# Optimization experiments

Measured on AMD Instinct MI355X. Metric: run time of the kernel, lower is better.

## Reference

```python
import jax, jax.numpy as jnp
import numpy as np

N_NODES = 100000
N_EDGES = 3200000
D_IN = 128
D_OUT = 128


def setup_inputs() -> dict:
    key = jax.random.key(0)
    k1, k2, k3, k4 = jax.random.split(key, 4)
    features = jax.random.normal(k1, (N_NODES, D_IN), dtype=jnp.float32)
    src = jax.random.randint(k2, (N_EDGES,), 0, N_NODES, dtype=jnp.int32)
    dst = jax.random.randint(k3, (N_EDGES,), 0, N_NODES, dtype=jnp.int32)
    # nn.Linear params (Kaiming-uniform-ish init scale)
    bound = 1.0 / np.sqrt(D_IN)
    W = jax.random.uniform(k4, (D_IN, D_OUT), dtype=jnp.float32, minval=-bound, maxval=bound)
    b = jnp.zeros((D_OUT,), dtype=jnp.float32)
    return {"features": features, "W": W, "b": b, "src": src, "dst": dst}


def reference(features, W, b, src, dst):
    # message: gather source node features per edge  [E, D_IN]
    msg = features[src]
    # mean_reduce: segment mean over in-edges per destination node
    summed = jax.ops.segment_sum(msg, dst, num_segments=N_NODES)
    deg = jax.ops.segment_sum(jnp.ones((msg.shape[0],), dtype=features.dtype), dst, num_segments=N_NODES)
    deg = deg[:, None]
    # DGL semantics: nodes with no incoming messages keep their original 'h'
    h = jnp.where(deg > 0, summed / jnp.maximum(deg, 1.0), features)
    # node_update: linear + activation applied to all nodes
    return jax.nn.relu(h @ W + b)
```

## Files before the change

kernel.cpp:

```cpp
#include <hip/hip_runtime.h>

#define N_NODES 100000
#define N_EDGES 3200000
#define D 128

#define BSHIFT 8
#define BSIZE  256
#define NBUCK  391
#define CAP    10240
#define PART_TILE 4096
#define NB_PART ((N_EDGES + PART_TILE - 1) / PART_TILE)
#define CPL 7
#define NSTRIPS (N_NODES / 16)
#define FUSE_GRID 1250

#define OFF_GCUR  0
#define OFF_DBASE 512
#define OFF_OFFS  1024
#define OFF_DEG   101024
#define OFF_CSR   201024
#define FEATB_OFF 13604096ULL
#define WPK_OFF   39204096ULL

typedef __attribute__((ext_vector_type(8))) short short8_t;
typedef __attribute__((ext_vector_type(4))) float f32x4;

__device__ __forceinline__ ushort f2bf(float x) {
    unsigned u = __float_as_uint(x);
    unsigned r = u + 0x7FFFu + ((u >> 16) & 1u);
    return (ushort)(r >> 16);
}
__device__ __forceinline__ float blo(unsigned v) { return __uint_as_float(v << 16); }
__device__ __forceinline__ float bhi(unsigned v) { return __uint_as_float(v & 0xFFFF0000u); }

__global__ __launch_bounds__(256) void gcn_cvt_kernel(
    const float* __restrict__ in, ushort* __restrict__ out, int n8)
{
    int i = blockIdx.x * 256 + threadIdx.x;
    if (i >= n8) return;
    const float4* p = (const float4*)in + (size_t)i * 2;
    float4 a = p[0], b = p[1];
    ushort4 r0 = make_ushort4(f2bf(a.x), f2bf(a.y), f2bf(a.z), f2bf(a.w));
    ushort4 r1 = make_ushort4(f2bf(b.x), f2bf(b.y), f2bf(b.z), f2bf(b.w));
    ushort4* q = (ushort4*)out + (size_t)i * 2;
    q[0] = r0;
    q[1] = r1;
}

__global__ __launch_bounds__(256) void gcn_wpack_kernel(
    const float* __restrict__ W, ushort* __restrict__ wpk)
{
    int tid = blockIdx.x * 256 + threadIdx.x;
    if (tid >= 32 * 64) return;
    int f = tid >> 6, l = tid & 63;
    int n4 = f >> 2, k4 = f & 3;
    int col = n4 * 16 + (l & 15);
    int kb  = k4 * 32 + ((l >> 4) << 3);
    ushort* q = wpk + (size_t)tid * 8;
    #pragma unroll
    for (int t = 0; t < 8; ++t) q[t] = f2bf(W[(kb + t) * D + col]);
}

__global__ void gcn_init_kernel(int* __restrict__ gcur)
{
    int t = blockIdx.x * 256 + threadIdx.x;
    if (t < NBUCK) gcur[t] = t * CAP;
}

__global__ __launch_bounds__(256) void gcn_part_kernel(
    const int* __restrict__ src, const int* __restrict__ dst,
    int* __restrict__ gcur, int* __restrict__ part)
{
    __shared__ int cnt[NBUCK];
    __shared__ int base[NBUCK];
    int t = threadIdx.x;
    for (int i = t; i < NBUCK; i += 256) cnt[i] = 0;
    __syncthreads();

    int eb = blockIdx.x * PART_TILE;
    int dv[PART_TILE / 256], sv[PART_TILE / 256];
    #pragma unroll
    for (int it = 0; it < PART_TILE / 256; ++it) {
        int e = eb + it * 256 + t;
        dv[it] = (e < N_EDGES) ? dst[e] : -1;
        sv[it] = (e < N_EDGES) ? src[e] : 0;
        if (dv[it] >= 0) atomicAdd(&cnt[dv[it] >> BSHIFT], 1);
    }
    __syncthreads();
    for (int i = t; i < NBUCK; i += 256) {
        int c = cnt[i];
        base[i] = c ? atomicAdd(&gcur[i], c) : 0;
        cnt[i] = 0;
    }
    __syncthreads();
    #pragma unroll
    for (int it = 0; it < PART_TILE / 256; ++it) {
        if (dv[it] >= 0) {
            int k  = dv[it] >> BSHIFT;
            int dl = dv[it] & (BSIZE - 1);
            int p  = base[k] + atomicAdd(&cnt[k], 1);
            part[p] = (dl << 17) | sv[it];
        }
    }
}

__global__ __launch_bounds__(64) void gcn_bscan_kernel(
    const int* __restrict__ gcur, int* __restrict__ dbase)
{
    int l = threadIdx.x;
    int v[CPL];
    int s = 0;
    #pragma unroll
    for (int j = 0; j < CPL; ++j) {
        int i = CPL * l + j;
        v[j] = (i < NBUCK) ? (gcur[i] - i * CAP) : 0;
        s += v[j];
    }
    int inc = s;
    #pragma unroll
    for (int d = 1; d < 64; d <<= 1) {
        int up = __shfl_up(inc, d, 64);
        if (l >= d) inc += up;
    }
    int run = inc - s;
    #pragma unroll
    for (int j = 0; j < CPL; ++j) {
        int i = CPL * l + j;
        if (i < NBUCK) dbase[i] = run;
        run += v[j];
    }
}

__global__ __launch_bounds__(256) void gcn_bfill_kernel(
    const int* __restrict__ gcur, const int* __restrict__ dbase,
    const int* __restrict__ part, int* __restrict__ csr,
    int* __restrict__ offs, int* __restrict__ deg)
{
    __shared__ int stage[CAP];
    __shared__ int ldeg[BSIZE];
    __shared__ int lcur[BSIZE];
    __shared__ int wsum[4];
    int k = blockIdx.x, t = threadIdx.x;
    int pb = k * CAP;
    int nE = gcur[k] - pb;
    if (nE > CAP) nE = CAP;
    int db = dbase[k];

    ldeg[t] = 0;
    __syncthreads();
    for (int i = t; i < nE; i += 256) {
        int pk = part[pb + i];
        stage[i] = pk;
        atomicAdd(&ldeg[pk >> 17], 1);
    }
    __syncthreads();

    int lane = t & 63, wid = t >> 6;
    int v = ldeg[t];
    int inc = v;
    #pragma unroll
    for (int d = 1; d < 64; d <<= 1) {
        int up = __shfl_up(inc, d, 64);
        if (lane >= d) inc += up;
    }
    if (lane == 63) wsum[wid] = inc;
    __syncthreads();
    if (t == 0) {
        int c = 0;
        #pragma unroll
        for (int w = 0; w < 4; ++w) { int x = wsum[w]; wsum[w] = c; c += x; }
    }
    __syncthreads();
    int excl = (inc - v) + wsum[wid];
    lcur[t] = excl;
    int node = (k << BSHIFT) + t;
    if (node < N_NODES) { offs[node] = db + excl; deg[node] = v; }
    __syncthreads();

    for (int i = t; i < nE; i += 256) {
        int pk = stage[i];
        int p = atomicAdd(&lcur[pk >> 17], 1);
        csr[db + p] = pk & 0x1FFFF;
    }
}

__global__ __launch_bounds__(256) void gcn_fused_kernel(
    const float* __restrict__ feat,
    const ushort* __restrict__ featb,
    const ushort* __restrict__ wpk,
    const float* __restrict__ bias,
    const int* __restrict__ offs,
    const int* __restrict__ deg,
    const int* __restrict__ csr,
    float* __restrict__ out)
{
    int t = threadIdx.x, lane = t & 63, w = t >> 6;

    short8_t wb[8];
    #pragma unroll
    for (int j = 0; j < 8; ++j)
        wb[j] = *(const short8_t*)(wpk + ((size_t)(w * 8 + j) * 64 + lane) * 8);
    float bj[2];
    bj[0] = bias[(2 * w) * 16 + (lane & 15)];
    bj[1] = bias[(2 * w + 1) * 16 + (lane & 15)];

    __shared__ ushort hlds[16 * 136];

    for (int s = blockIdx.x; s < NSTRIPS; s += FUSE_GRID) {
        int m0 = s * 16;
        __syncthreads();

        #pragma unroll
        for (int i = 0; i < 4; ++i) {
            int r = m0 + w * 4 + i;
            int beg = offs[r], dg = deg[r];
            float s0 = 0.0f, s1 = 0.0f;
            if (dg == 0) {
                float2 f2 = *(const float2*)(feat + (size_t)r * D + lane * 2);
                s0 = f2.x; s1 = f2.y;
            } else {
                int p = beg, e = beg + dg;
                for (; p + 4 <= e; p += 4) {
                    int i0 = csr[p], i1 = csr[p + 1], i2 = csr[p + 2], i3 = csr[p + 3];
                    unsigned v0 = *(const unsigned*)(featb + ((size_t)i0 << 7) + lane * 2);
                    unsigned v1 = *(const unsigned*)(featb + ((size_t)i1 << 7) + lane * 2);
                    unsigned v2 = *(const unsigned*)(featb + ((size_t)i2 << 7) + lane * 2);
                    unsigned v3 = *(const unsigned*)(featb + ((size_t)i3 << 7) + lane * 2);
                    s0 += blo(v0) + blo(v1) + blo(v2) + blo(v3);
                    s1 += bhi(v0) + bhi(v1) + bhi(v2) + bhi(v3);
                }
                for (; p < e; ++p) {
                    unsigned v = *(const unsigned*)(featb + ((size_t)csr[p] << 7) + lane * 2);
                    s0 += blo(v); s1 += bhi(v);
                }
                float inv = 1.0f / (float)dg;
                s0 *= inv; s1 *= inv;
            }
            unsigned pk = ((unsigned)f2bf(s1) << 16) | (unsigned)f2bf(s0);
            *(unsigned*)(&hlds[(w * 4 + i) * 136 + lane * 2]) = pk;
        }
        __syncthreads();

        short8_t a[4];
        #pragma unroll
        for (int k4 = 0; k4 < 4; ++k4)
            a[k4] = *(const short8_t*)(&hlds[(lane & 15) * 136 + k4 * 32 + ((lane >> 4) << 3)]);

        #pragma unroll
        for (int nt = 0; nt < 2; ++nt) {
            f32x4 acc = { bj[nt], bj[nt], bj[nt], bj[nt] };
            #pragma unroll
            for (int k4 = 0; k4 < 4; ++k4)
                acc = __builtin_amdgcn_mfma_f32_16x16x32_bf16(a[k4], wb[nt * 4 + k4], acc, 0, 0, 0);
            int col  = (2 * w + nt) * 16 + (lane & 15);
            int rowb = m0 + ((lane >> 4) << 2);
            #pragma unroll
            for (int rr = 0; rr < 4; ++rr)
                out[(size_t)(rowb + rr) * D + col] = fmaxf(acc[rr], 0.0f);
        }
    }
}

extern "C" void kernel_launch(void* const* d_in, const int* in_sizes, int n_in,
                              void* d_out, int out_size, void* d_ws, size_t ws_size,
                              hipStream_t stream) {
    const float* feat = (const float*)d_in[0];
    const float* W    = (const float*)d_in[1];
    const float* bias = (const float*)d_in[2];
    const int*   src  = (const int*)d_in[3];
    const int*   dst  = (const int*)d_in[4];
    float* out = (float*)d_out;

    int* ib     = (int*)d_ws;
    int* gcur   = ib + OFF_GCUR;
    int* dbase  = ib + OFF_DBASE;
    int* offs   = ib + OFF_OFFS;
    int* deg    = ib + OFF_DEG;
    int* csr    = ib + OFF_CSR;
    ushort* featb = (ushort*)((char*)d_ws + FEATB_OFF);
    ushort* wpk   = (ushort*)((char*)d_ws + WPK_OFF);
    int* part = (int*)d_out;

    {
        int n8 = N_NODES * D / 8;
        gcn_cvt_kernel<<<(n8 + 255) / 256, 256, 0, stream>>>(feat, featb, n8);
    }
    gcn_wpack_kernel<<<8, 256, 0, stream>>>(W, wpk);
    gcn_init_kernel<<<2, 256, 0, stream>>>(gcur);
    gcn_part_kernel<<<NB_PART, 256, 0, stream>>>(src, dst, gcur, part);
    gcn_bscan_kernel<<<1, 64, 0, stream>>>(gcur, dbase);
    gcn_bfill_kernel<<<NBUCK, 256, 0, stream>>>(gcur, dbase, part, csr, offs, deg);
    gcn_fused_kernel<<<FUSE_GRID, 256, 0, stream>>>(feat, featb, wpk, bias, offs, deg, csr, out);
}
```

Measured before the change: 355.9 us.

## Stage partition and CSR fill writes in LDS for coalesced stores; unroll gather by 8

```diff
diff --git a/kernel.cpp b/kernel.cpp
--- a/kernel.cpp
+++ b/kernel.cpp
@@ -7,12 +7,12 @@
 #define BSHIFT 8
 #define BSIZE  256
 #define NBUCK  391
-#define CAP    10240
+#define CAP    9216
 #define PART_TILE 4096
 #define NB_PART ((N_EDGES + PART_TILE - 1) / PART_TILE)
 #define CPL 7
 #define NSTRIPS (N_NODES / 16)
-#define FUSE_GRID 1250
+#define FUSE_GRID 2084
 
 #define OFF_GCUR  0
 #define OFF_DBASE 512
@@ -72,35 +72,76 @@
     int* __restrict__ gcur, int* __restrict__ part)
 {
     __shared__ int cnt[NBUCK];
-    __shared__ int base[NBUCK];
+    __shared__ int lbase[NBUCK + 1];
+    __shared__ int gbase[NBUCK];
+    __shared__ int stage[PART_TILE];
+    __shared__ ushort sbuck[PART_TILE];
+
     int t = threadIdx.x;
+    int eb = blockIdx.x * PART_TILE;
+    int nT = N_EDGES - eb; if (nT > PART_TILE) nT = PART_TILE;
+
     for (int i = t; i < NBUCK; i += 256) cnt[i] = 0;
     __syncthreads();
 
-    int eb = blockIdx.x * PART_TILE;
-    int dv[PART_TILE / 256], sv[PART_TILE / 256];
     #pragma unroll
     for (int it = 0; it < PART_TILE / 256; ++it) {
-        int e = eb + it * 256 + t;
-        dv[it] = (e < N_EDGES) ? dst[e] : -1;
-        sv[it] = (e < N_EDGES) ? src[e] : 0;
-        if (dv[it] >= 0) atomicAdd(&cnt[dv[it] >> BSHIFT], 1);
-    }
-    __syncthreads();
+        int e = it * 256 + t;
+        if (e < nT) atomicAdd(&cnt[dst[eb + e] >> BSHIFT], 1);
+    }
+    __syncthreads();
+
+    if (t < 64) {
+        int v[CPL];
+        int s = 0;
+        #pragma unroll
+        for (int j = 0; j < CPL; ++j) {
+            int i = t * CPL + j;
+            v[j] = (i < NBUCK) ? cnt[i] : 0;
+            s += v[j];
+        }
+        int inc = s;
+        #pragma unroll
+        for (int d = 1; d < 64; d <<= 1) {
+            int up = __shfl_up(inc, d, 64);
+            if (t >= d) inc += up;
+        }
+        int run = inc - s;
+        #pragma unroll
+        for (int j = 0; j < CPL; ++j) {
+            int i = t * CPL + j;
+            if (i < NBUCK) lbase[i] = run;
+            run += v[j];
+        }
+        if (t == 63) lbase[NBUCK] = run;
+    }
+    __syncthreads();
+
     for (int i = t; i < NBUCK; i += 256) {
-        int c = cnt[i];
-        base[i] = c ? atomicAdd(&gcur[i], c) : 0;
+        int c = lbase[i + 1] - lbase[i];
+        gbase[i] = c ? atomicAdd(&gcur[i], c) : 0;
         cnt[i] = 0;
     }
     __syncthreads();
+
     #pragma unroll
     for (int it = 0; it < PART_TILE / 256; ++it) {
-        if (dv[it] >= 0) {
-            int k  = dv[it] >> BSHIFT;
-            int dl = dv[it] & (BSIZE - 1);
-            int p  = base[k] + atomicAdd(&cnt[k], 1);
-            part[p] = (dl << 17) | sv[it];
-        }
+        int e = it * 256 + t;
+        if (e < nT) {
+            int dvv = dst[eb + e];
+            int svv = src[eb + e];
+            int b  = dvv >> BSHIFT;
+            int dl = dvv & (BSIZE - 1);
+            int pos = lbase[b] + atomicAdd(&cnt[b], 1);
+            stage[pos] = (dl << 17) | svv;
+            sbuck[pos] = (ushort)b;
+        }
+    }
+    __syncthreads();
+
+    for (int i = t; i < nT; i += 256) {
+        int b = sbuck[i];
+        part[gbase[b] + (i - lbase[b])] = stage[i];
     }
 }
 
@@ -137,6 +178,7 @@
     int* __restrict__ offs, int* __restrict__ deg)
 {
     __shared__ int stage[CAP];
+    __shared__ int stage2[CAP];
     __shared__ int ldeg[BSIZE];
     __shared__ int lcur[BSIZE];
     __shared__ int wsum[4];
@@ -180,8 +222,11 @@
     for (int i = t; i < nE; i += 256) {
         int pk = stage[i];
         int p = atomicAdd(&lcur[pk >> 17], 1);
-        csr[db + p] = pk & 0x1FFFF;
-    }
+        stage2[p] = pk & 0x1FFFF;
+    }
+    __syncthreads();
+
+    for (int i = t; i < nE; i += 256) csr[db + i] = stage2[i];
 }
 
 __global__ __launch_bounds__(256) void gcn_fused_kernel(
@@ -220,6 +265,22 @@
                 s0 = f2.x; s1 = f2.y;
             } else {
                 int p = beg, e = beg + dg;
+                for (; p + 8 <= e; p += 8) {
+                    int i0 = csr[p],     i1 = csr[p + 1], i2 = csr[p + 2], i3 = csr[p + 3];
+                    int i4 = csr[p + 4], i5 = csr[p + 5], i6 = csr[p + 6], i7 = csr[p + 7];
+                    unsigned v0 = *(const unsigned*)(featb + ((size_t)i0 << 7) + lane * 2);
+                    unsigned v1 = *(const unsigned*)(featb + ((size_t)i1 << 7) + lane * 2);
+                    unsigned v2 = *(const unsigned*)(featb + ((size_t)i2 << 7) + lane * 2);
+                    unsigned v3 = *(const unsigned*)(featb + ((size_t)i3 << 7) + lane * 2);
+                    unsigned v4 = *(const unsigned*)(featb + ((size_t)i4 << 7) + lane * 2);
+                    unsigned v5 = *(const unsigned*)(featb + ((size_t)i5 << 7) + lane * 2);
+                    unsigned v6 = *(const unsigned*)(featb + ((size_t)i6 << 7) + lane * 2);
+                    unsigned v7 = *(const unsigned*)(featb + ((size_t)i7 << 7) + lane * 2);
+                    s0 += blo(v0) + blo(v1) + blo(v2) + blo(v3);
+                    s1 += bhi(v0) + bhi(v1) + bhi(v2) + bhi(v3);
+                    s0 += blo(v4) + blo(v5) + blo(v6) + blo(v7);
+                    s1 += bhi(v4) + bhi(v5) + bhi(v6) + bhi(v7);
+                }
                 for (; p + 4 <= e; p += 4) {
                     int i0 = csr[p], i1 = csr[p + 1], i2 = csr[p + 2], i3 = csr[p + 3];
                     unsigned v0 = *(const unsigned*)(featb + ((size_t)i0 << 7) + lane * 2);
```

Result: faster. 319.8 us (-10.1%).
